# Optimization experiments

Hardware: AMD Instinct MI355X
Metric: run time of the kernel (lower is better)

Reference implementation:

```python
import jax, jax.numpy as jnp
import numpy as np

SCALE = 1.0 / 4.0      # alpha / dim
MULTIPLIER = 1.0

def _act(h):
    return jax.nn.gelu(h, approximate=False)  # torch nn.GELU(approximate='none')

def setup_inputs() -> dict:
    key = jax.random.key(0)
    ks = jax.random.split(key, 9)
    B, T, D = 64, 77, 768
    N, R = 1024, 4
    return {
        "x":     jax.random.normal(ks[0], (B, T, D), jnp.float32),
        "W_org": jax.random.normal(ks[1], (D, D), jnp.float32) * 0.02,
        "b_org": jax.random.normal(ks[2], (D,), jnp.float32) * 0.02,
        "w1":    jax.random.normal(ks[3], (N, D, R), jnp.float32) * 0.02,
        "b1":    jax.random.normal(ks[4], (N, R), jnp.float32) * 0.02,
        "mid_w": jax.random.normal(ks[5], (N, R, R), jnp.float32) * 0.02,
        "mid_b": jax.random.normal(ks[6], (N, R), jnp.float32) * 0.02,
        "w_out": jax.random.normal(ks[7], (N, R, D), jnp.float32) * 0.02,
        "b_out": jax.random.normal(ks[8], (N, D), jnp.float32) * 0.02,
    }

def reference(x, W_org, b_org, w1, b1, mid_w, mid_b, w_out, b_out):
    # per-concept low-rank MLP: h in [B, T, N, R]
    h = jnp.einsum('btd,ndh->btnh', x, w1) + b1[None, None]
    h = _act(h)
    # repeated 'h' in 'nhh' takes the diagonal of mid_w (elementwise scale),
    # exactly matching torch.einsum semantics in the source.
    h = jnp.einsum('btnh,nhh->btnh', h, mid_w) + mid_b[None, None]
    h = _act(h)
    # fuse out-projection with sum over concepts: sum_n (h_n @ w_out_n) + sum_n b_out_n
    up = jnp.einsum('btnh,nhd->btd', h, w_out) + jnp.sum(b_out, axis=0)
    org = x @ W_org.T + b_org
    return org + up * (MULTIPLIER * SCALE)
```

## Files before the change

kernel.cpp:

```cpp
#include <hip/hip_runtime.h>
#include <hip/hip_bf16.h>

#define M_TOK 4928
#define M_PAD 5120
#define D_DIM 768
#define NR    4096
#define K_CAT 4864
#define KT_ALL 152

typedef __bf16 bf16;
typedef __attribute__((ext_vector_type(8))) __bf16 bf16x8;
typedef __attribute__((ext_vector_type(4))) float f32x4;
typedef __attribute__((address_space(1))) uint32_t gu32;
typedef __attribute__((address_space(3))) uint32_t su32;

__device__ __forceinline__ float gelu_fast(float v) {
  float p = v * v;
  float u = v * fmaf(0.07135481283f, p, 1.595769122f);
  float e = __expf(-u);
  return v * __builtin_amdgcn_rcpf(1.0f + e);
}

__device__ __forceinline__ int xcd_swizzle(int orig, int nwg) {
  const int q = nwg >> 3, r = nwg & 7;
  const int x = orig & 7, rest = orig >> 3;
  return (x < r ? x * (q + 1) : r * (q + 1) + (x - r) * q) + rest;
}


__global__ __launch_bounds__(256) void k_prep_x(const float* __restrict__ x,
                                                bf16* __restrict__ Xb) {
  int idx = (blockIdx.x * 256 + threadIdx.x) * 4;
  if (idx >= M_PAD * D_DIM) return;
  int m = idx / D_DIM;
  union { uint2 u; bf16 h[4]; } o;
  if (m < M_TOK) {
    float4 v = *(const float4*)(x + idx);
    o.h[0] = (bf16)v.x; o.h[1] = (bf16)v.y; o.h[2] = (bf16)v.z; o.h[3] = (bf16)v.w;
  } else {
    o.h[0] = o.h[1] = o.h[2] = o.h[3] = (bf16)0.0f;
  }
  *(uint2*)(Xb + idx) = o.u;
}

__global__ __launch_bounds__(256) void k_prep_w1t(const float* __restrict__ w1,
                                                  bf16* __restrict__ W1t) {
  int idx = (blockIdx.x * 256 + threadIdx.x) * 4;
  if (idx >= NR * D_DIM) return;
  int j = idx / D_DIM, d0 = idx % D_DIM;
  int n = j >> 2, r = j & 3;
  const float* src = w1 + n * (D_DIM * 4) + r;
  union { uint2 u; bf16 h[4]; } o;
#pragma unroll
  for (int i = 0; i < 4; ++i) o.h[i] = (bf16)src[(d0 + i) * 4];
  *(uint2*)(W1t + idx) = o.u;
}

__global__ __launch_bounds__(256) void k_prep_w2t_t(const float* __restrict__ w_out,
                                                    bf16* __restrict__ W2t) {
  __shared__ float S[64 * 65];
  const int bk = blockIdx.x & 63, bd = blockIdx.x >> 6;
  const int k0 = bk * 64, d0 = bd * 64;
  const int tr = threadIdx.x >> 4;
  const int tc = (threadIdx.x & 15) * 4;
#pragma unroll
  for (int p = 0; p < 4; ++p) {
    const int kr = tr + p * 16;
    float4 v = *(const float4*)(w_out + (size_t)(k0 + kr) * D_DIM + d0 + tc);
    S[kr * 65 + tc + 0] = v.x; S[kr * 65 + tc + 1] = v.y;
    S[kr * 65 + tc + 2] = v.z; S[kr * 65 + tc + 3] = v.w;
  }
  __syncthreads();
#pragma unroll
  for (int p = 0; p < 4; ++p) {
    const int dr = tr + p * 16;
    union { uint2 u; bf16 h[4]; } o;
#pragma unroll
    for (int i = 0; i < 4; ++i) o.h[i] = (bf16)(0.25f * S[(tc + i) * 65 + dr]);
    *(uint2*)(W2t + (size_t)(d0 + dr) * K_CAT + k0 + tc) = o.u;
  }
}

__global__ __launch_bounds__(256) void k_prep_w2t_org(const float* __restrict__ W_org,
                                                      bf16* __restrict__ W2t) {
  int idx = (blockIdx.x * 256 + threadIdx.x) * 4;
  if (idx >= D_DIM * D_DIM) return;
  int d = idx / D_DIM, c = idx % D_DIM;
  float4 v = *(const float4*)(W_org + idx);
  union { uint2 u; bf16 h[4]; } o;
  o.h[0] = (bf16)v.x; o.h[1] = (bf16)v.y; o.h[2] = (bf16)v.z; o.h[3] = (bf16)v.w;
  *(uint2*)(W2t + (size_t)d * K_CAT + NR + c) = o.u;
}

__global__ __launch_bounds__(256) void k_bias_partial(const float* __restrict__ b_out,
                                                      float* __restrict__ partial) {
  int b = blockIdx.x;
  for (int d = threadIdx.x; d < D_DIM; d += 256) {
    float s = 0.0f;
    for (int n = b * 32; n < b * 32 + 32; ++n) s += b_out[n * D_DIM + d];
    partial[b * D_DIM + d] = s;
  }
}

__global__ __launch_bounds__(256) void k_bias_final(const float* __restrict__ partial,
                                                    const float* __restrict__ b_org,
                                                    float* __restrict__ bias_total) {
  int d = blockIdx.x * 256 + threadIdx.x;
  if (d >= D_DIM) return;
  float s = 0.0f;
#pragma unroll
  for (int b = 0; b < 32; ++b) s += partial[b * D_DIM + d];
  bias_total[d] = b_org[d] + 0.25f * s;
}


__device__ __forceinline__ int swz_slot(int kg, int lr) {
  return (kg ^ ((lr >> 1) & 3)) << 3;
}

__device__ __forceinline__ void stage_tile4(const bf16* g, int ld, int row0, int col0,
                                            bf16* lds) {
  const int lane = threadIdx.x & 63;
  const int wave = threadIdx.x >> 6;
  const int src_slot = (lane & 3) ^ ((lane >> 3) & 3);
#pragma unroll
  for (int c = 0; c < 2; ++c) {
    const int chunk = wave * 2 + c;
    const int row = row0 + chunk * 16 + (lane >> 2);
    const bf16* gp = g + (size_t)row * ld + col0 + (src_slot << 3);
    __builtin_amdgcn_global_load_lds((gu32*)gp, (su32*)(lds + chunk * 512), 16, 0, 0);
  }
}

__device__ __forceinline__ void stage_unit8(const bf16* g, int ld, int row0, int col0,
                                            bf16* lds) {
  const int lane = threadIdx.x & 63;
  const int wave = threadIdx.x >> 6;
  const int src_slot = (lane & 3) ^ ((lane >> 3) & 3);
#pragma unroll
  for (int c = 0; c < 2; ++c) {
    const int chunk = wave * 2 + c;
    const int row = row0 + chunk * 16 + (lane >> 2);
    const bf16* gp = g + (size_t)row * ld + col0 + (src_slot << 3);
    __builtin_amdgcn_global_load_lds((gu32*)gp, (su32*)(lds + chunk * 512), 16, 0, 0);
  }
}

#define TILE_E (128 * 32)

#define PIPE_LOOP(KT0, KT1, STAGE_PAIR, BODY)                                   \
  {                                                                             \
    STAGE_PAIR(KT0, 0);                                                         \
    STAGE_PAIR((KT0) + 1, 1);                                                   \
    int ra = 0;                                                                 \
    for (int kt = (KT0); kt < (KT1); ++kt) {                                    \
      if (kt + 1 < (KT1)) { asm volatile("s_waitcnt vmcnt(4)" ::: "memory"); }  \
      else                { asm volatile("s_waitcnt vmcnt(0)" ::: "memory"); }  \
      asm volatile("s_barrier" ::: "memory");                                   \
      const int rs = ra + 2 >= 3 ? ra - 1 : ra + 2;                             \
      BODY(ra);                                                                 \
      if (kt + 2 < (KT1)) STAGE_PAIR(kt + 2, rs);                               \
      ra = (ra + 1 == 3) ? 0 : ra + 1;                                          \
    }                                                                           \
  }

__global__ __launch_bounds__(256) void k_gemm1(const bf16* __restrict__ Xb,
                                               const bf16* __restrict__ W1t,
                                               bf16* __restrict__ H2,
                                               const float* __restrict__ b1,
                                               const float* __restrict__ midw,
                                               const float* __restrict__ midb) {
  __shared__ bf16 As[3][TILE_E];
  __shared__ bf16 Bs[3][TILE_E];
  const int wgid = xcd_swizzle(blockIdx.x, 40 * 32);
  const int bmt = wgid >> 5;
  const int bnt = wgid & 31;
  const int m0 = bmt * 128, n0 = bnt * 128;
  const int lane = threadIdx.x & 63;
  const int wave = threadIdx.x >> 6;
  const int wm = wave >> 1, wn = wave & 1;
  const int lr = lane & 15, kg = lane >> 4;
  const int slot = swz_slot(kg, lr);

  f32x4 acc[4][4];
#pragma unroll
  for (int i = 0; i < 4; ++i)
#pragma unroll
    for (int j = 0; j < 4; ++j) acc[i][j] = (f32x4)(0.0f);

#define G1_STAGE(kt, buf)                                   \
  {                                                         \
    stage_tile4(Xb, D_DIM, m0, (kt) * 32, As[(buf)]);       \
    stage_tile4(W1t, D_DIM, n0, (kt) * 32, Bs[(buf)]);      \
  }
#define G1_BODY(cur)                                                         \
  {                                                                          \
    bf16x8 a[4], b[4];                                                       \
    _Pragma("unroll") for (int i = 0; i < 4; ++i)                            \
      a[i] = *(const bf16x8*)(As[(cur)] + (wm * 64 + i * 16 + lr) * 32 + slot); \
    _Pragma("unroll") for (int j = 0; j < 4; ++j)                            \
      b[j] = *(const bf16x8*)(Bs[(cur)] + (wn * 64 + j * 16 + lr) * 32 + slot); \
    _Pragma("unroll") for (int i = 0; i < 4; ++i)                            \
      _Pragma("unroll") for (int j = 0; j < 4; ++j)                          \
        acc[i][j] = __builtin_amdgcn_mfma_f32_16x16x32_bf16(a[i], b[j], acc[i][j], 0, 0, 0); \
  }

  PIPE_LOOP(0, 24, G1_STAGE, G1_BODY)
#undef G1_STAGE
#undef G1_BODY

#pragma unroll
  for (int j = 0; j < 4; ++j) {
    const int col = n0 + wn * 64 + j * 16 + lr;
    const float b1v = b1[col];
    const float mdv = midw[(col >> 2) * 16 + (col & 3) * 5];
    const float mbv = midb[col];
#pragma unroll
    for (int i = 0; i < 4; ++i) {
      const int r0 = m0 + wm * 64 + i * 16 + kg * 4;
#pragma unroll
      for (int rr = 0; rr < 4; ++rr) {
        float h = acc[i][j][rr] + b1v;
        h = gelu_fast(h);
        h = h * mdv + mbv;
        h = gelu_fast(h);
        H2[(size_t)(r0 + rr) * NR + col] = (bf16)h;
      }
    }
  }
}


#define ENGINE(KT0, KT1, STAGE_A, STAGE_B)                                      \
  {                                                                             \
    STAGE_A((KT0) + 0, 0); STAGE_B((KT0) + 0, 0);                               \
    STAGE_A((KT0) + 1, 1); STAGE_B((KT0) + 1, 1);                               \
    STAGE_A((KT0) + 2, 2); STAGE_B((KT0) + 2, 2);                               \
    asm volatile("s_waitcnt vmcnt(8)" ::: "memory");                            \
    asm volatile("s_barrier" ::: "memory");                                     \
    for (int t = (KT0); t < (KT1); ++t) {                                       \
      const int s  = (t - (KT0)) & 3;                                           \
      const int st = (t - (KT0) + 3) & 3;                                       \
      const bool more = (t + 3 < (KT1));                                        \
      bf16x8 a[8], b[4];                                                        \
      _Pragma("unroll") for (int i = 0; i < 4; ++i)                             \
        a[i] = *(const bf16x8*)(As[s] + aBase + i * 512);                       \
      _Pragma("unroll") for (int j = 0; j < 4; ++j)                             \
        b[j] = *(const bf16x8*)(Bs[s] + bBase + j * 512);                       \
      if (more) { STAGE_A(t + 3, st); }                                         \
      asm volatile("s_barrier" ::: "memory");                                   \
      __builtin_amdgcn_s_setprio(1);                                            \
      _Pragma("unroll") for (int i = 0; i < 4; ++i)                             \
        _Pragma("unroll") for (int j = 0; j < 4; ++j)                           \
          acc[i][j] = __builtin_amdgcn_mfma_f32_16x16x32_bf16(a[i], b[j], acc[i][j], 0, 0, 0); \
      __builtin_amdgcn_s_setprio(0);                                            \
      asm volatile("s_barrier" ::: "memory");                                   \
      _Pragma("unroll") for (int i = 0; i < 4; ++i)                             \
        a[4 + i] = *(const bf16x8*)(As[s] + aBase + 2048 + i * 512);            \
      if (more) { STAGE_B(t + 3, st); }                                         \
      {                                                                         \
        int ahead = ((KT1) - 1) - (t + 1);                                      \
        if (ahead >= 2)      { asm volatile("s_waitcnt vmcnt(8)" ::: "memory"); } \
        else if (ahead == 1) { asm volatile("s_waitcnt vmcnt(4)" ::: "memory"); } \
        else                 { asm volatile("s_waitcnt vmcnt(0)" ::: "memory"); } \
      }                                                                         \
      asm volatile("s_barrier" ::: "memory");                                   \
      __builtin_amdgcn_s_setprio(1);                                            \
      _Pragma("unroll") for (int i = 0; i < 4; ++i)                             \
        _Pragma("unroll") for (int j = 0; j < 4; ++j)                           \
          acc[4 + i][j] = __builtin_amdgcn_mfma_f32_16x16x32_bf16(a[4 + i], b[j], acc[4 + i][j], 0, 0, 0); \
      __builtin_amdgcn_s_setprio(0);                                            \
      asm volatile("s_barrier" ::: "memory");                                   \
    }                                                                           \
  }

template <int SPLITS>
__global__ __launch_bounds__(512) void k_gemm2(const bf16* __restrict__ H2,
                                               const bf16* __restrict__ Xb,
                                               const bf16* __restrict__ W2t,
                                               void* __restrict__ outp,
                                               const float* __restrict__ bias) {
  __shared__ bf16 As[4][8192];
  __shared__ bf16 Bs[4][8192];
  const int nwg = 20 * 3 * SPLITS;
  const int wgid = xcd_swizzle(blockIdx.x, nwg);
  const int bmt = wgid / (3 * SPLITS);
  const int rem = wgid % (3 * SPLITS);
  const int ks  = rem / 3;
  const int bnt = rem % 3;
  const int m0 = bmt * 256, n0 = bnt * 256;
  const int lane = threadIdx.x & 63;
  const int wave = threadIdx.x >> 6;
  const int wm = wave >> 2, wn = wave & 3;
  const int lr = lane & 15, kg = lane >> 4;
  const int slotE = swz_slot(kg, lr);
  const int aBase = (wm * 128 + lr) * 32 + slotE;
  const int bBase = (wn * 64 + lr) * 32 + slotE;
  constexpr int KT_PER = KT_ALL / SPLITS;
  const int kt0 = ks * KT_PER, kt1 = kt0 + KT_PER;

  f32x4 acc[8][4];
#pragma unroll
  for (int i = 0; i < 8; ++i)
#pragma unroll
    for (int j = 0; j < 4; ++j) acc[i][j] = (f32x4)(0.0f);

#define G2_SA(kt, buf)                                                  \
  {                                                                     \
    const int k0s = (kt) * 32;                                          \
    if (k0s < NR) stage_unit8(H2, NR, m0, k0s, As[(buf)]);              \
    else          stage_unit8(Xb, D_DIM, m0, k0s - NR, As[(buf)]);      \
  }
#define G2_SB(kt, buf) stage_unit8(W2t, K_CAT, n0, (kt) * 32, Bs[(buf)])
  ENGINE(kt0, kt1, G2_SA, G2_SB)
#undef G2_SA
#undef G2_SB

  if (SPLITS > 1) {
    bf16* dst = (bf16*)outp + (size_t)ks * M_TOK * D_DIM;
#pragma unroll
    for (int j = 0; j < 4; ++j) {
      const int col = n0 + wn * 64 + j * 16 + lr;
#pragma unroll
      for (int i = 0; i < 8; ++i) {
        const int r0 = m0 + wm * 128 + i * 16 + kg * 4;
#pragma unroll
        for (int rr = 0; rr < 4; ++rr) {
          const int row = r0 + rr;
          if (row < M_TOK) dst[(size_t)row * D_DIM + col] = (bf16)acc[i][j][rr];
        }
      }
    }
  } else {
    float* dst = (float*)outp;
#pragma unroll
    for (int j = 0; j < 4; ++j) {
      const int col = n0 + wn * 64 + j * 16 + lr;
      const float bv = bias[col];
#pragma unroll
      for (int i = 0; i < 8; ++i) {
        const int r0 = m0 + wm * 128 + i * 16 + kg * 4;
#pragma unroll
        for (int rr = 0; rr < 4; ++rr) {
          const int row = r0 + rr;
          if (row < M_TOK) dst[(size_t)row * D_DIM + col] = acc[i][j][rr] + bv;
        }
      }
    }
  }
}

template <int SPLITS>
__global__ __launch_bounds__(256) void k_reduce(const bf16* __restrict__ padd,
                                                const float* __restrict__ bias,
                                                float* __restrict__ out) {
  int idx = (blockIdx.x * 256 + threadIdx.x) * 4;
  if (idx >= M_TOK * D_DIM) return;
  float4 s = *(const float4*)(bias + (idx % D_DIM));
#pragma unroll
  for (int p = 0; p < SPLITS; ++p) {
    union { uint2 u; bf16 h[4]; } v;
    v.u = *(const uint2*)(padd + (size_t)p * M_TOK * D_DIM + idx);
    s.x += (float)v.h[0]; s.y += (float)v.h[1];
    s.z += (float)v.h[2]; s.w += (float)v.h[3];
  }
  *(float4*)(out + idx) = s;
}


extern "C" void kernel_launch(void* const* d_in, const int* in_sizes, int n_in,
                              void* d_out, int out_size, void* d_ws, size_t ws_size,
                              hipStream_t stream) {
  const float* x     = (const float*)d_in[0];
  const float* W_org = (const float*)d_in[1];
  const float* b_org = (const float*)d_in[2];
  const float* w1    = (const float*)d_in[3];
  const float* b1    = (const float*)d_in[4];
  const float* mid_w = (const float*)d_in[5];
  const float* mid_b = (const float*)d_in[6];
  const float* w_out = (const float*)d_in[7];
  const float* b_out = (const float*)d_in[8];
  float* out = (float*)d_out;

  bf16* Xb   = (bf16*)d_ws;
  bf16* W1t  = Xb  + (size_t)M_PAD * D_DIM;
  bf16* W2t  = W1t + (size_t)NR * D_DIM;
  bf16* H2   = W2t + (size_t)D_DIM * K_CAT;
  float* bias    = (float*)(H2 + (size_t)M_PAD * NR);
  float* partial = bias + 1024;
  bf16* padd     = (bf16*)(partial + 32 * D_DIM);

  const size_t base_bytes = (size_t)((char*)padd - (char*)d_ws);
  const size_t per_split  = (size_t)M_TOK * D_DIM * sizeof(bf16);
  int S = 1;
  if (ws_size >= base_bytes + 4 * per_split)      S = 4;
  else if (ws_size >= base_bytes + 2 * per_split) S = 2;

  k_prep_x     <<<(M_PAD * D_DIM / 4) / 256, 256, 0, stream>>>(x, Xb);
  k_prep_w1t   <<<(NR * D_DIM / 4) / 256, 256, 0, stream>>>(w1, W1t);
  k_prep_w2t_t <<<64 * 12, 256, 0, stream>>>(w_out, W2t);
  k_prep_w2t_org<<<(D_DIM * D_DIM / 4 + 255) / 256, 256, 0, stream>>>(W_org, W2t);
  k_bias_partial<<<32, 256, 0, stream>>>(b_out, partial);
  k_bias_final  <<<3, 256, 0, stream>>>(partial, b_org, bias);

  k_gemm1<<<40 * 32, 256, 0, stream>>>(Xb, W1t, H2, b1, mid_w, mid_b);

  const int red_grid = (M_TOK * D_DIM / 4 + 255) / 256;
  if (S == 4) {
    k_gemm2<4><<<20 * 3 * 4, 512, 0, stream>>>(H2, Xb, W2t, padd, bias);
    k_reduce<4><<<red_grid, 256, 0, stream>>>(padd, bias, out);
  } else if (S == 2) {
    k_gemm2<2><<<20 * 3 * 2, 512, 0, stream>>>(H2, Xb, W2t, padd, bias);
    k_reduce<2><<<red_grid, 256, 0, stream>>>(padd, bias, out);
  } else {
    k_gemm2<1><<<20 * 3, 512, 0, stream>>>(H2, Xb, W2t, out, bias);
  }
}
```

Measured before the change: 136.6 us.

## Vectorize GEMM epilogues via swapped MFMA operands, cheapen GELU, trim grid

Swaps the MFMA A/B operands so each lane holds four consecutive columns of one row. This lets the gemm1 and gemm2 epilogues write packed 8-byte bf16 and 16-byte fp32 stores instead of scalar strided ones. It also replaces the tanh-style GELU with a sigmoid approximation x*sigmoid(1.702x) using exp2, and precomputes the mid_w diagonal into a small buffer read with float4 loads. The w1 transpose now uses float4 reads and 16-byte writes, and the gemm1 grid drops the padded 40th row tile. The cruder GELU approximation risks accuracy, and the shrunken grid relies on M_TOK fitting in 39 tiles.

```diff
diff --git a/kernel.cpp b/kernel.cpp
--- a/kernel.cpp
+++ b/kernel.cpp
@@ -14,10 +14,8 @@
 typedef __attribute__((address_space(1))) uint32_t gu32;
 typedef __attribute__((address_space(3))) uint32_t su32;
 
-__device__ __forceinline__ float gelu_fast(float v) {
-  float p = v * v;
-  float u = v * fmaf(0.07135481283f, p, 1.595769122f);
-  float e = __expf(-u);
+__device__ __forceinline__ float act_fast(float v) {
+  float e = __builtin_amdgcn_exp2f(v * -2.4554677f);
   return v * __builtin_amdgcn_rcpf(1.0f + e);
 }
 
@@ -45,15 +43,20 @@
 
 __global__ __launch_bounds__(256) void k_prep_w1t(const float* __restrict__ w1,
                                                   bf16* __restrict__ W1t) {
-  int idx = (blockIdx.x * 256 + threadIdx.x) * 4;
-  if (idx >= NR * D_DIM) return;
-  int j = idx / D_DIM, d0 = idx % D_DIM;
-  int n = j >> 2, r = j & 3;
-  const float* src = w1 + n * (D_DIM * 4) + r;
-  union { uint2 u; bf16 h[4]; } o;
-#pragma unroll
-  for (int i = 0; i < 4; ++i) o.h[i] = (bf16)src[(d0 + i) * 4];
-  *(uint2*)(W1t + idx) = o.u;
+  int gid = blockIdx.x * 256 + threadIdx.x;
+  int n = gid / 96, oct = gid % 96;
+  const float4* src = (const float4*)w1 + (size_t)n * D_DIM + oct * 8;
+  bf16x8 rows[4];
+#pragma unroll
+  for (int d = 0; d < 8; ++d) {
+    float4 v = src[d];
+    rows[0][d] = (bf16)v.x; rows[1][d] = (bf16)v.y;
+    rows[2][d] = (bf16)v.z; rows[3][d] = (bf16)v.w;
+  }
+  size_t base = (size_t)n * 4 * D_DIM + oct * 8;
+#pragma unroll
+  for (int r = 0; r < 4; ++r)
+    *(bf16x8*)(W1t + base + (size_t)r * D_DIM) = rows[r];
 }
 
 __global__ __launch_bounds__(256) void k_prep_w2t_t(const float* __restrict__ w_out,
@@ -102,15 +105,23 @@
   }
 }
 
-__global__ __launch_bounds__(256) void k_bias_final(const float* __restrict__ partial,
-                                                    const float* __restrict__ b_org,
-                                                    float* __restrict__ bias_total) {
-  int d = blockIdx.x * 256 + threadIdx.x;
-  if (d >= D_DIM) return;
-  float s = 0.0f;
-#pragma unroll
-  for (int b = 0; b < 32; ++b) s += partial[b * D_DIM + d];
-  bias_total[d] = b_org[d] + 0.25f * s;
+__global__ __launch_bounds__(256) void k_bias_final2(const float* __restrict__ partial,
+                                                     const float* __restrict__ b_org,
+                                                     const float* __restrict__ mid_w,
+                                                     float* __restrict__ bias_total,
+                                                     float* __restrict__ diag) {
+  int b = blockIdx.x;
+  if (b < 3) {
+    int d = b * 256 + threadIdx.x;
+    if (d >= D_DIM) return;
+    float s = 0.0f;
+#pragma unroll
+    for (int p = 0; p < 32; ++p) s += partial[p * D_DIM + d];
+    bias_total[d] = b_org[d] + 0.25f * s;
+  } else {
+    int j = (b - 3) * 256 + threadIdx.x;
+    diag[j] = mid_w[(j >> 2) * 16 + (j & 3) * 5];
+  }
 }
 
 
@@ -168,11 +179,11 @@
                                                const bf16* __restrict__ W1t,
                                                bf16* __restrict__ H2,
                                                const float* __restrict__ b1,
-                                               const float* __restrict__ midw,
+                                               const float* __restrict__ diag,
                                                const float* __restrict__ midb) {
   __shared__ bf16 As[3][TILE_E];
   __shared__ bf16 Bs[3][TILE_E];
-  const int wgid = xcd_swizzle(blockIdx.x, 40 * 32);
+  const int wgid = xcd_swizzle(blockIdx.x, 39 * 32);
   const int bmt = wgid >> 5;
   const int bnt = wgid & 31;
   const int m0 = bmt * 128, n0 = bnt * 128;
@@ -202,7 +213,7 @@
       b[j] = *(const bf16x8*)(Bs[(cur)] + (wn * 64 + j * 16 + lr) * 32 + slot); \
     _Pragma("unroll") for (int i = 0; i < 4; ++i)                            \
       _Pragma("unroll") for (int j = 0; j < 4; ++j)                          \
-        acc[i][j] = __builtin_amdgcn_mfma_f32_16x16x32_bf16(a[i], b[j], acc[i][j], 0, 0, 0); \
+        acc[i][j] = __builtin_amdgcn_mfma_f32_16x16x32_bf16(b[j], a[i], acc[i][j], 0, 0, 0); \
   }
 
   PIPE_LOOP(0, 24, G1_STAGE, G1_BODY)
@@ -211,21 +222,20 @@
 
 #pragma unroll
   for (int j = 0; j < 4; ++j) {
-    const int col = n0 + wn * 64 + j * 16 + lr;
-    const float b1v = b1[col];
-    const float mdv = midw[(col >> 2) * 16 + (col & 3) * 5];
-    const float mbv = midb[col];
+    const int jcb = n0 + wn * 64 + j * 16 + kg * 4;
+    const float4 b1v = *(const float4*)(b1 + jcb);
+    const float4 dgv = *(const float4*)(diag + jcb);
+    const float4 mbv = *(const float4*)(midb + jcb);
 #pragma unroll
     for (int i = 0; i < 4; ++i) {
-      const int r0 = m0 + wm * 64 + i * 16 + kg * 4;
-#pragma unroll
-      for (int rr = 0; rr < 4; ++rr) {
-        float h = acc[i][j][rr] + b1v;
-        h = gelu_fast(h);
-        h = h * mdv + mbv;
-        h = gelu_fast(h);
-        H2[(size_t)(r0 + rr) * NR + col] = (bf16)h;
-      }
+      const int mr = m0 + wm * 64 + i * 16 + lr;
+      union { uint2 u; bf16 h[4]; } o;
+      float h;
+      h = act_fast(acc[i][j][0] + b1v.x); o.h[0] = (bf16)act_fast(h * dgv.x + mbv.x);
+      h = act_fast(acc[i][j][1] + b1v.y); o.h[1] = (bf16)act_fast(h * dgv.y + mbv.y);
+      h = act_fast(acc[i][j][2] + b1v.z); o.h[2] = (bf16)act_fast(h * dgv.z + mbv.z);
+      h = act_fast(acc[i][j][3] + b1v.w); o.h[3] = (bf16)act_fast(h * dgv.w + mbv.w);
+      *(uint2*)(H2 + (size_t)mr * NR + jcb) = o.u;
     }
   }
 }
@@ -252,7 +262,7 @@
       __builtin_amdgcn_s_setprio(1);                                            \
       _Pragma("unroll") for (int i = 0; i < 4; ++i)                             \
         _Pragma("unroll") for (int j = 0; j < 4; ++j)                           \
-          acc[i][j] = __builtin_amdgcn_mfma_f32_16x16x32_bf16(a[i], b[j], acc[i][j], 0, 0, 0); \
+          acc[i][j] = __builtin_amdgcn_mfma_f32_16x16x32_bf16(b[j], a[i], acc[i][j], 0, 0, 0); \
       __builtin_amdgcn_s_setprio(0);                                            \
       asm volatile("s_barrier" ::: "memory");                                   \
       _Pragma("unroll") for (int i = 0; i < 4; ++i)                             \
@@ -268,7 +278,7 @@
       __builtin_amdgcn_s_setprio(1);                                            \
       _Pragma("unroll") for (int i = 0; i < 4; ++i)                             \
         _Pragma("unroll") for (int j = 0; j < 4; ++j)                           \
-          acc[4 + i][j] = __builtin_amdgcn_mfma_f32_16x16x32_bf16(a[4 + i], b[j], acc[4 + i][j], 0, 0, 0); \
+          acc[4 + i][j] = __builtin_amdgcn_mfma_f32_16x16x32_bf16(b[j], a[4 + i], acc[4 + i][j], 0, 0, 0); \
       __builtin_amdgcn_s_setprio(0);                                            \
       asm volatile("s_barrier" ::: "memory");                                   \
     }                                                                           \
@@ -320,14 +330,15 @@
     bf16* dst = (bf16*)outp + (size_t)ks * M_TOK * D_DIM;
 #pragma unroll
     for (int j = 0; j < 4; ++j) {
-      const int col = n0 + wn * 64 + j * 16 + lr;
+      const int cb = n0 + wn * 64 + j * 16 + kg * 4;
 #pragma unroll
       for (int i = 0; i < 8; ++i) {
-        const int r0 = m0 + wm * 128 + i * 16 + kg * 4;
-#pragma unroll
-        for (int rr = 0; rr < 4; ++rr) {
-          const int row = r0 + rr;
-          if (row < M_TOK) dst[(size_t)row * D_DIM + col] = (bf16)acc[i][j][rr];
+        const int mr = m0 + wm * 128 + i * 16 + lr;
+        if (mr < M_TOK) {
+          union { uint2 u; bf16 h[4]; } o;
+          o.h[0] = (bf16)acc[i][j][0]; o.h[1] = (bf16)acc[i][j][1];
+          o.h[2] = (bf16)acc[i][j][2]; o.h[3] = (bf16)acc[i][j][3];
+          *(uint2*)(dst + (size_t)mr * D_DIM + cb) = o.u;
         }
       }
     }
@@ -335,15 +346,14 @@
     float* dst = (float*)outp;
 #pragma unroll
     for (int j = 0; j < 4; ++j) {
-      const int col = n0 + wn * 64 + j * 16 + lr;
-      const float bv = bias[col];
+      const int cb = n0 + wn * 64 + j * 16 + kg * 4;
+      const f32x4 bv = *(const f32x4*)(bias + cb);
 #pragma unroll
       for (int i = 0; i < 8; ++i) {
-        const int r0 = m0 + wm * 128 + i * 16 + kg * 4;
-#pragma unroll
-        for (int rr = 0; rr < 4; ++rr) {
-          const int row = r0 + rr;
-          if (row < M_TOK) dst[(size_t)row * D_DIM + col] = acc[i][j][rr] + bv;
+        const int mr = m0 + wm * 128 + i * 16 + lr;
+        if (mr < M_TOK) {
+          f32x4 o = acc[i][j] + bv;
+          *(f32x4*)(dst + (size_t)mr * D_DIM + cb) = o;
         }
       }
     }
@@ -388,7 +398,8 @@
   bf16* H2   = W2t + (size_t)D_DIM * K_CAT;
   float* bias    = (float*)(H2 + (size_t)M_PAD * NR);
   float* partial = bias + 1024;
-  bf16* padd     = (bf16*)(partial + 32 * D_DIM);
+  float* diag    = partial + 32 * D_DIM;
+  bf16* padd     = (bf16*)(diag + NR);
 
   const size_t base_bytes = (size_t)((char*)padd - (char*)d_ws);
   const size_t per_split  = (size_t)M_TOK * D_DIM * sizeof(bf16);
@@ -397,13 +408,13 @@
   else if (ws_size >= base_bytes + 2 * per_split) S = 2;
 
   k_prep_x     <<<(M_PAD * D_DIM / 4) / 256, 256, 0, stream>>>(x, Xb);
-  k_prep_w1t   <<<(NR * D_DIM / 4) / 256, 256, 0, stream>>>(w1, W1t);
+  k_prep_w1t   <<<384, 256, 0, stream>>>(w1, W1t);
   k_prep_w2t_t <<<64 * 12, 256, 0, stream>>>(w_out, W2t);
   k_prep_w2t_org<<<(D_DIM * D_DIM / 4 + 255) / 256, 256, 0, stream>>>(W_org, W2t);
   k_bias_partial<<<32, 256, 0, stream>>>(b_out, partial);
-  k_bias_final  <<<3, 256, 0, stream>>>(partial, b_org, bias);
-
-  k_gemm1<<<40 * 32, 256, 0, stream>>>(Xb, W1t, H2, b1, mid_w, mid_b);
+  k_bias_final2 <<<19, 256, 0, stream>>>(partial, b_org, mid_w, bias, diag);
+
+  k_gemm1<<<39 * 32, 256, 0, stream>>>(Xb, W1t, H2, b1, diag, mid_b);
 
   const int red_grid = (M_TOK * D_DIM / 4 + 255) / 256;
   if (S == 4) {
```

Result: no change. 135.6 us (-0.7%).
